# Optimization experiments

Hardware: AMD Instinct MI355X
Metric: run time of the kernel (lower is better)

The kernel has to match this reference:

```python
import jax, jax.numpy as jnp
import numpy as np

B, IN, E, D = 131072, 113, 4, 8
H1, H2 = 256, 113          # expert MLP dims [256, 113]
T1, T2 = 256, 128          # tower dims: fcn_dims = [256, 128]
EPS = 1e-5


def _bn(x, gamma, beta):
    # Training-mode BatchNorm1d over the batch axis (axis 0), biased variance.
    mean = jnp.mean(x, axis=0, keepdims=True)
    var = jnp.var(x, axis=0, keepdims=True)
    return (x - mean) * jax.lax.rsqrt(var + EPS) * gamma + beta


def setup_inputs() -> dict:
    key = jax.random.key(0)
    ks = jax.random.split(key, 24)
    s = 0.02
    return {
        "emb": jax.random.normal(ks[0], (B, IN), jnp.float32),
        "domain_id": jax.random.randint(ks[1], (B,), 0, D, jnp.int64),
        # experts (stacked over E): Linear->BN->ReLU, Linear->BN->ReLU
        "We1": jax.random.normal(ks[2], (E, IN, H1), jnp.float32) * s,
        "be1": jnp.zeros((E, H1), jnp.float32),
        "eg1": jnp.ones((E, H1), jnp.float32),
        "eb1": jnp.zeros((E, H1), jnp.float32),
        "We2": jax.random.normal(ks[3], (E, H1, H2), jnp.float32) * s,
        "be2": jnp.zeros((E, H2), jnp.float32),
        "eg2": jnp.ones((E, H2), jnp.float32),
        "eb2": jnp.zeros((E, H2), jnp.float32),
        # gates (stacked over D): Linear(IN, E) + softmax
        "Wg": jax.random.normal(ks[4], (D, IN, E), jnp.float32) * s,
        "bg": jnp.zeros((D, E), jnp.float32),
        # domain towers (stacked over D): 113->256 BN ReLU -> 128 BN ReLU -> 1, sigmoid
        "Wt1": jax.random.normal(ks[5], (D, H2, T1), jnp.float32) * s,
        "bt1": jnp.zeros((D, T1), jnp.float32),
        "tg1": jnp.ones((D, T1), jnp.float32),
        "tb1": jnp.zeros((D, T1), jnp.float32),
        "Wt2": jax.random.normal(ks[6], (D, T1, T2), jnp.float32) * s,
        "bt2": jnp.zeros((D, T2), jnp.float32),
        "tg2": jnp.ones((D, T2), jnp.float32),
        "tb2": jnp.zeros((D, T2), jnp.float32),
        "Wt3": jax.random.normal(ks[7], (D, T2, 1), jnp.float32) * s,
        "bt3": jnp.zeros((D, 1), jnp.float32),
    }


def reference(emb, We1, be1, eg1, eb1, We2, be2, eg2, eb2, Wg, bg,
              Wt1, bt1, tg1, tb1, Wt2, bt2, tg2, tb2, Wt3, bt3, domain_id):
    # experts, batched over E: [B, E, H1] -> [B, E, H2]
    h = jax.nn.relu(_bn(jnp.einsum('bi,eio->beo', emb, We1) + be1, eg1, eb1))
    fea = jax.nn.relu(_bn(jnp.einsum('beo,eoc->bec', h, We2) + be2, eg2, eb2))
    # gates, batched over D: [B, D, E] softmax over experts
    gates = jax.nn.softmax(jnp.einsum('bi,die->bde', emb, Wg) + bg, axis=-1)
    # soft mixture: [B, D, H2]
    task = jnp.einsum('bde,bec->bdc', gates, fea)
    # domain towers, batched over D (original computes every tower on the full batch)
    t1 = jax.nn.relu(_bn(jnp.einsum('bdc,dco->bdo', task, Wt1) + bt1, tg1, tb1))
    t2 = jax.nn.relu(_bn(jnp.einsum('bdo,doh->bdh', t1, Wt2) + bt2, tg2, tb2))
    out = jax.nn.sigmoid(jnp.einsum('bdh,dho->bdo', t2, Wt3) + bt3)[..., 0]  # [B, D]
    # masked select: final[b] = out[b, domain_id[b]]
    final = jnp.take_along_axis(out, domain_id[:, None], axis=1)[:, 0]  # [B]
    return final
```

## Files before the change

### kernel.cpp

```cpp
#include <hip/hip_runtime.h>
#include <hip/hip_bf16.h>


#define B_ROWS 131072
#define EPS_BN 1e-5f

typedef unsigned short bf_t;
typedef unsigned int u32;
typedef short bf16x8 __attribute__((ext_vector_type(8)));
typedef float f32x4  __attribute__((ext_vector_type(4)));

__device__ __forceinline__ float bf2f(bf_t u) { return __uint_as_float(((u32)u) << 16); }
__device__ __forceinline__ bf_t f2bf(float f) {
    u32 x = __float_as_uint(f);
    u32 r = x + 0x7FFFu + ((x >> 16) & 1u);
    return (bf_t)(r >> 16);
}

__global__ __launch_bounds__(256)
void prep_w(const float* __restrict__ W, bf_t* __restrict__ WT,
            int G, int K, int N, int CPAD, int KP)
{
    long total = (long)G * CPAD * KP;
    for (long idx = (long)blockIdx.x * 256 + threadIdx.x; idx < total;
         idx += (long)gridDim.x * 256) {
        int kk = (int)(idx % KP);
        long t = idx / KP;
        int c = (int)(t % CPAD);
        int g = (int)(t / CPAD);
        float v = 0.f;
        if (kk < K && c < N) v = W[((long)g * K + kk) * N + c];
        WT[idx] = f2bf(v);
    }
}

__global__ __launch_bounds__(256)
void prep_emb(const float* __restrict__ emb, bf_t* __restrict__ embB)
{
    const long total = (long)B_ROWS * 16;
    for (long idx = (long)blockIdx.x * 256 + threadIdx.x; idx < total;
         idx += (long)gridDim.x * 256) {
        long b = idx >> 4;
        int c0 = (int)(idx & 15) << 3;
        u32 o[4];
#pragma unroll
        for (int p = 0; p < 4; ++p) {
            int c = c0 + p * 2;
            float f0 = (c < 113)     ? emb[b * 113 + c]     : 0.f;
            float f1 = (c + 1 < 113) ? emb[b * 113 + c + 1] : 0.f;
            o[p] = (u32)f2bf(f0) | ((u32)f2bf(f1) << 16);
        }
        *(uint4*)&embB[b * 128 + c0] = make_uint4(o[0], o[1], o[2], o[3]);
    }
}

template<int XMODE, int NTILE, int KPAD, bool SEL>
__global__ __launch_bounds__(512, 1)
void gemm_big(const bf_t* __restrict__ X, int xrs, int Kreal,
              const float* __restrict__ gates,
              const float* __restrict__ statS, const float* __restrict__ statQ,
              const float* __restrict__ gamma, const float* __restrict__ beta, int nchIn,
              const bf_t* __restrict__ WT,
              const float* __restrict__ bias, int N,
              bf_t* __restrict__ Y, int yrs, int ycol0,
              const int* __restrict__ dom, int dsel,
              float* __restrict__ oSum, float* __restrict__ oSq)
{
    constexpr int NCH  = KPAD / 128;
    constexpr int WSTR = KPAD + 8;
    constexpr int XSTR = 136;
    constexpr int WCW  = NTILE / 4;
    constexpr int CF   = WCW / 16;
    constexpr int TPB  = 4;
    constexpr int NIT  = TPB * NCH;

    __shared__ bf_t  WsL[NTILE * WSTR];
    __shared__ bf_t  XsL[2][128 * XSTR];
    __shared__ float scS[512], shS[512];

    const int tid  = threadIdx.x;
    const int lane = tid & 63;
    const int w    = tid >> 6;
    const int wr   = w >> 2, wc = w & 3;
    const int g    = lane >> 4, lr = lane & 15;
    const int sr   = tid >> 2;
    const int so   = (tid & 3) << 5;
    const long tb0 = (long)blockIdx.x * TPB;

#pragma unroll
    for (int i = 0; i < NTILE * KPAD / 8 / 512; ++i) {
        int idx = tid + i * 512;
        int col = idx / (KPAD / 8);
        int ks  = (idx % (KPAD / 8)) * 8;
        *(uint4*)&WsL[col * WSTR + ks] = *(const uint4*)&WT[(long)col * KPAD + ks];
    }
    if (XMODE != 0) {
        for (int c = tid; c < nchIn; c += 512) {
            float m = statS[c] * (1.f / B_ROWS);
            float v = statQ[c] * (1.f / B_ROWS) - m * m;
            float s = gamma[c] * rsqrtf(v + EPS_BN);
            scS[c] = s;
            shS[c] = beta[c] - m * s;
        }
    }
    float bj[CF];
#pragma unroll
    for (int ci = 0; ci < CF; ++ci) {
        int col = wc * WCW + ci * 16 + lr;
        bj[ci] = (col < N) ? bias[col] : 0.f;
    }
    __syncthreads();

    f32x4 acc[4][CF];
#pragma unroll
    for (int ri = 0; ri < 4; ++ri)
#pragma unroll
        for (int ci = 0; ci < CF; ++ci) acc[ri][ci] = (f32x4){0.f, 0.f, 0.f, 0.f};
    float csum[CF], csq[CF];
#pragma unroll
    for (int ci = 0; ci < CF; ++ci) { csum[ci] = 0.f; csq[ci] = 0.f; }

    auto issue4 = [&](int it, uint4* r) {
        int t = it / NCH, ck = (it % NCH) << 7;
        long row = (tb0 + t) * 128 + sr;
#pragma unroll
        for (int j = 0; j < 4; ++j)
            r[j] = *(const uint4*)&X[row * (long)xrs + ck + so + j * 8];
    };
    auto twrite = [&](int it, const uint4* r) {
        bf_t* dst = &XsL[it & 1][sr * XSTR + so];
        if (XMODE == 0) {
#pragma unroll
            for (int j = 0; j < 4; ++j) *(uint4*)(dst + j * 8) = r[j];
        } else {
            int ck = (it % NCH) << 7;
#pragma unroll
            for (int j = 0; j < 4; ++j) {
                u32 q[4] = {r[j].x, r[j].y, r[j].z, r[j].w};
                u32 o[4];
#pragma unroll
                for (int p = 0; p < 4; ++p) {
                    int k0 = ck + so + j * 8 + p * 2;
                    float f0 = fmaxf(bf2f((bf_t)(q[p] & 0xffffu)) * scS[k0] + shS[k0], 0.f);
                    float f1 = fmaxf(bf2f((bf_t)(q[p] >> 16)) * scS[k0 + 1] + shS[k0 + 1], 0.f);
                    o[p] = (u32)f2bf(f0) | ((u32)f2bf(f1) << 16);
                }
                *(uint4*)(dst + j * 8) = make_uint4(o[0], o[1], o[2], o[3]);
            }
        }
    };
    auto stage2 = [&](int it) {
        long row = (tb0 + it) * 128 + sr;
        float4 g4 = *(const float4*)&gates[row * 32];
        uint4 r[16];
#pragma unroll
        for (int j = 0; j < 4; ++j)
#pragma unroll
            for (int e = 0; e < 4; ++e)
                r[j * 4 + e] = *(const uint4*)&X[row * 480 + e * 120 + so + j * 8];
        float ge[4] = {g4.x, g4.y, g4.z, g4.w};
        bf_t* dst = &XsL[it & 1][sr * XSTR + so];
#pragma unroll
        for (int j = 0; j < 4; ++j) {
            float vv[8];
#pragma unroll
            for (int p = 0; p < 8; ++p) vv[p] = 0.f;
#pragma unroll
            for (int e = 0; e < 4; ++e) {
                u32 q[4] = {r[j * 4 + e].x, r[j * 4 + e].y, r[j * 4 + e].z, r[j * 4 + e].w};
#pragma unroll
                for (int p = 0; p < 8; ++p) {
                    int k = so + j * 8 + p;
                    if (k < Kreal) {
                        float f = bf2f((bf_t)((q[p >> 1] >> ((p & 1) * 16)) & 0xffffu));
                        int ch = e * 113 + k;
                        f = fmaxf(f * scS[ch] + shS[ch], 0.f);
                        vv[p] = fmaf(ge[e], f, vv[p]);
                    }
                }
            }
            u32 o[4];
#pragma unroll
            for (int p = 0; p < 4; ++p)
                o[p] = (u32)f2bf(vv[p * 2]) | ((u32)f2bf(vv[p * 2 + 1]) << 16);
            *(uint4*)(dst + j * 8) = make_uint4(o[0], o[1], o[2], o[3]);
        }
    };
    auto do_mfma = [&](int it) {
        const bf_t* xb = XsL[it & 1];
        const int ck = (it % NCH) << 7;
#pragma unroll
        for (int kt = 0; kt < 4; ++kt) {
            bf16x8 af[4];
#pragma unroll
            for (int ri = 0; ri < 4; ++ri)
                af[ri] = *(const bf16x8*)&xb[(wr * 64 + ri * 16 + lr) * XSTR + kt * 32 + g * 8];
#pragma unroll
            for (int ci = 0; ci < CF; ++ci) {
                bf16x8 bf8 = *(const bf16x8*)&WsL[(wc * WCW + ci * 16 + lr) * WSTR + ck + kt * 32 + g * 8];
#pragma unroll
                for (int ri = 0; ri < 4; ++ri)
                    acc[ri][ci] = __builtin_amdgcn_mfma_f32_16x16x32_bf16(
                        af[ri], bf8, acc[ri][ci], 0, 0, 0);
            }
        }
    };
    auto epi = [&](int t) {
        const long row0 = (tb0 + t) * 128;
#pragma unroll
        for (int ci = 0; ci < CF; ++ci) {
            int col = wc * WCW + ci * 16 + lr;
            bool cv = col < N;
#pragma unroll
            for (int ri = 0; ri < 4; ++ri) {
#pragma unroll
                for (int reg = 0; reg < 4; ++reg) {
                    long row = row0 + wr * 64 + ri * 16 + g * 4 + reg;
                    float y = acc[ri][ci][reg] + bj[ci];
                    csum[ci] += y;
                    csq[ci]  += y * y;
                    bool st = cv;
                    if (SEL) st = st && (dom[row] == dsel);
                    if (st) Y[row * (long)yrs + ycol0 + col] = f2bf(y);
                    acc[ri][ci][reg] = 0.f;
                }
            }
        }
    };

    if (XMODE != 2) {
        uint4 rA[4], rB[4];
        issue4(0, rA);
#pragma unroll 1
        for (int ip = 0; ip < NIT; ip += 2) {
            if (ip + 1 < NIT) issue4(ip + 1, rB);
            twrite(ip, rA);
            __syncthreads();
            do_mfma(ip);
            if ((ip % NCH) == NCH - 1) epi(ip / NCH);
            if (ip + 2 < NIT) issue4(ip + 2, rA);
            twrite(ip + 1, rB);
            __syncthreads();
            do_mfma(ip + 1);
            if (((ip + 1) % NCH) == NCH - 1) epi((ip + 1) / NCH);
        }
    } else {
#pragma unroll 1
        for (int it = 0; it < NIT; ++it) {
            stage2(it);
            __syncthreads();
            do_mfma(it);
            epi(it);
        }
    }

#pragma unroll
    for (int ci = 0; ci < CF; ++ci) {
        float s = csum[ci], q = csq[ci];
        s += __shfl_xor(s, 16); s += __shfl_xor(s, 32);
        q += __shfl_xor(q, 16); q += __shfl_xor(q, 32);
        if (lane < 16) {
            int col = wc * WCW + ci * 16 + lane;
            if (col < N) {
                atomicAdd(&oSum[col], s);
                atomicAdd(&oSq[col], q);
            }
        }
    }
}

__global__ __launch_bounds__(256)
void gates_kernel(const float* __restrict__ emb, const float* __restrict__ Wg,
                  const float* __restrict__ bg, float* __restrict__ gates)
{
    __shared__ float embS[64][116];
    __shared__ float WgS[8 * 113 * 4];
    __shared__ float bgS[32];
    const int tid = threadIdx.x;
    const int r0 = blockIdx.x << 6;

    for (int idx = tid; idx < 64 * 113; idx += 256) {
        int rr = idx / 113, kk = idx - rr * 113;
        embS[rr][kk] = emb[(long)(r0 + rr) * 113 + kk];
    }
    for (int idx = tid; idx < 8 * 113 * 4; idx += 256) WgS[idx] = Wg[idx];
    if (tid < 32) bgS[tid] = bg[tid];
    __syncthreads();

    const int q = tid & 3;
    const int r = tid >> 2;
#pragma unroll
    for (int p = 0; p < 2; ++p) {
        int d = q + p * 4;
        float lg[4] = {bgS[d * 4 + 0], bgS[d * 4 + 1], bgS[d * 4 + 2], bgS[d * 4 + 3]};
        for (int k = 0; k < 113; ++k) {
            float x = embS[r][k];
            const float* wp = &WgS[(d * 113 + k) * 4];
#pragma unroll
            for (int e = 0; e < 4; ++e) lg[e] = fmaf(x, wp[e], lg[e]);
        }
        float m = fmaxf(fmaxf(lg[0], lg[1]), fmaxf(lg[2], lg[3]));
        float ex[4], s = 0.f;
#pragma unroll
        for (int e = 0; e < 4; ++e) { ex[e] = expf(lg[e] - m); s += ex[e]; }
        float inv = 1.f / s;
        *(float4*)&gates[(long)(r0 + r) * 32 + d * 4] =
            make_float4(ex[0] * inv, ex[1] * inv, ex[2] * inv, ex[3] * inv);
    }
}

__global__ __launch_bounds__(256)
void final_kernel(const bf_t* __restrict__ Y4d, const int* __restrict__ dom,
                  const float* __restrict__ s4sum, const float* __restrict__ s4sq,
                  const float* __restrict__ g4, const float* __restrict__ b4,
                  const float* __restrict__ w3, const float* __restrict__ b3,
                  int d, float* __restrict__ out)
{
    __shared__ float sc[128], sh[128], wS[128];
    const int tid = threadIdx.x;
    if (tid < 128) {
        float m = s4sum[tid] * (1.f / B_ROWS);
        float v = s4sq[tid] * (1.f / B_ROWS) - m * m;
        float s = g4[tid] * rsqrtf(v + EPS_BN);
        sc[tid] = s;
        sh[tid] = b4[tid] - m * s;
        wS[tid] = w3[tid];
    }
    __syncthreads();
    const float bb = b3[0];
    for (long b = (long)blockIdx.x * 256 + tid; b < B_ROWS; b += (long)gridDim.x * 256) {
        if ((dom[b] & 7) == d) {
            const bf_t* yp = Y4d + b * 128;
            float acc = bb;
            for (int c = 0; c < 128; c += 8) {
                uint4 raw = *(const uint4*)(yp + c);
                u32 w4[4] = {raw.x, raw.y, raw.z, raw.w};
#pragma unroll
                for (int j = 0; j < 8; ++j) {
                    float f = bf2f((bf_t)((w4[j >> 1] >> ((j & 1) * 16)) & 0xffffu));
                    float h = fmaxf(f * sc[c + j] + sh[c + j], 0.f);
                    acc = fmaf(h, wS[c + j], acc);
                }
            }
            out[b] = 1.f / (1.f + expf(-acc));
        }
    }
}

extern "C" void kernel_launch(void* const* d_in, const int* in_sizes, int n_in,
                              void* d_out, int out_size, void* d_ws, size_t ws_size,
                              hipStream_t stream)
{
    const float* emb = (const float*)d_in[0];
    const int*   dom = (const int*)d_in[1];
    const float* We1 = (const float*)d_in[2];
    const float* be1 = (const float*)d_in[3];
    const float* eg1 = (const float*)d_in[4];
    const float* eb1 = (const float*)d_in[5];
    const float* We2 = (const float*)d_in[6];
    const float* be2 = (const float*)d_in[7];
    const float* eg2 = (const float*)d_in[8];
    const float* eb2 = (const float*)d_in[9];
    const float* Wg  = (const float*)d_in[10];
    const float* bg  = (const float*)d_in[11];
    const float* Wt1 = (const float*)d_in[12];
    const float* bt1 = (const float*)d_in[13];
    const float* tg1 = (const float*)d_in[14];
    const float* tb1 = (const float*)d_in[15];
    const float* Wt2 = (const float*)d_in[16];
    const float* bt2 = (const float*)d_in[17];
    const float* tg2 = (const float*)d_in[18];
    const float* tb2 = (const float*)d_in[19];
    const float* Wt3 = (const float*)d_in[20];
    const float* bt3 = (const float*)d_in[21];
    float* out = (float*)d_out;

    char* ws = (char*)d_ws;
    bf_t*  Y2    = (bf_t*)(ws);
    float* gates = (float*)(ws + 125829120LL);
    bf_t*  Yx    = (bf_t*)(ws + 142606336LL);
    bf_t*  Y4    = (bf_t*)(ws + 209715200LL);
    float* S     = (float*)(ws + 243269632LL);
    bf_t*  WTa   = (bf_t*)(ws + 243306496LL);

    bf_t* embB = Y4;
    bf_t* We1T = WTa;
    bf_t* We2T = We1T + 131072;
    bf_t* Wt1T = We2T + 131072;
    bf_t* Wt2T = Wt1T + 262144;

    float* S1s = S;           float* S1q = S1s + 1024;
    float* S2s = S1q + 1024;  float* S2q = S2s + 452;
    float* S3s = S2q + 452;   float* S3q = S3s + 2048;
    float* S4s = S3q + 2048;  float* S4q = S4s + 1024;

    hipMemsetAsync(S, 0, 9096 * sizeof(float), stream);

    prep_w<<<512, 256, 0, stream>>>(We1, We1T, 4, 113, 256, 256, 128);
    prep_w<<<512, 256, 0, stream>>>(We2, We2T, 4, 256, 113, 128, 256);
    prep_w<<<1024, 256, 0, stream>>>(Wt1, Wt1T, 8, 113, 256, 256, 128);
    prep_w<<<1024, 256, 0, stream>>>(Wt2, Wt2T, 8, 256, 128, 128, 256);
    prep_emb<<<2048, 256, 0, stream>>>(emb, embB);

    gates_kernel<<<2048, 256, 0, stream>>>(emb, Wg, bg, gates);

    for (int e = 0; e < 4; ++e) {
        gemm_big<0, 256, 128, false><<<256, 512, 0, stream>>>(
            embB, 128, 128,
            nullptr, nullptr, nullptr, nullptr, nullptr, 0,
            We1T + (long)e * 32768,
            be1 + e * 256, 256,
            Yx, 256, 0, nullptr, 0, S1s + e * 256, S1q + e * 256);
        gemm_big<1, 128, 256, false><<<256, 512, 0, stream>>>(
            Yx, 256, 256,
            nullptr, S1s + e * 256, S1q + e * 256, eg1 + e * 256, eb1 + e * 256, 256,
            We2T + (long)e * 32768,
            be2 + e * 113, 113,
            Y2, 480, e * 120, nullptr, 0, S2s + e * 113, S2q + e * 113);
    }

    for (int d = 0; d < 8; ++d) {
        gemm_big<2, 256, 128, false><<<256, 512, 0, stream>>>(
            Y2, 480, 113,
            gates + d * 4, S2s, S2q, eg2, eb2, 452,
            Wt1T + (long)d * 32768,
            bt1 + d * 256, 256,
            Yx, 256, 0, nullptr, 0, S3s + d * 256, S3q + d * 256);
        gemm_big<1, 128, 256, true><<<256, 512, 0, stream>>>(
            Yx, 256, 256,
            nullptr, S3s + d * 256, S3q + d * 256, tg1 + d * 256, tb1 + d * 256, 256,
            Wt2T + (long)d * 32768,
            bt2 + d * 128, 128,
            Y4, 128, 0, dom, d, S4s + d * 128, S4q + d * 128);
        final_kernel<<<1024, 256, 0, stream>>>(
            Y4, dom, S4s + d * 128, S4q + d * 128,
            tg2 + d * 128, tb2 + d * 128, Wt3 + d * 128, bt3 + d, d, out);
    }

    (void)in_sizes; (void)n_in; (void)out_size; (void)ws_size;
}
```

Measured before the change: 1.788 ms.

## Keep GEMM weight fragments in registers and XOR-swizzle the activation LDS tile

Each thread now loads its B-operand weight fragments for the whole K range into registers once per block, instead of staging the weight tile in shared memory and re-reading it for every MFMA step. The activation tile in LDS drops its padded stride and uses an XOR swizzle on 16-byte chunks to avoid bank conflicts. This removes the weight LDS traffic and shrinks LDS usage. In exchange it raises register pressure a lot, since CF*KT bf16x8 fragments stay live, which may cause spills for the wider NOUT/KPAD instances.

```diff
diff --git a/kernel.cpp b/kernel.cpp
--- a/kernel.cpp
+++ b/kernel.cpp
@@ -54,28 +54,26 @@
     }
 }
 
-template<int XMODE, int NTILE, int KPAD, bool SEL>
+template<int XMODE, int NOUT, int KPAD, bool SEL>
 __global__ __launch_bounds__(512, 1)
 void gemm_big(const bf_t* __restrict__ X, int xrs, int Kreal,
               const float* __restrict__ gates,
               const float* __restrict__ statS, const float* __restrict__ statQ,
               const float* __restrict__ gamma, const float* __restrict__ beta, int nchIn,
               const bf_t* __restrict__ WT,
-              const float* __restrict__ bias, int N,
+              const float* __restrict__ bias, int Nvalid,
               bf_t* __restrict__ Y, int yrs, int ycol0,
               const int* __restrict__ dom, int dsel,
               float* __restrict__ oSum, float* __restrict__ oSq)
 {
-    constexpr int NCH  = KPAD / 128;
-    constexpr int WSTR = KPAD + 8;
-    constexpr int XSTR = 136;
-    constexpr int WCW  = NTILE / 4;
-    constexpr int CF   = WCW / 16;
-    constexpr int TPB  = 4;
-    constexpr int NIT  = TPB * NCH;
-
-    __shared__ bf_t  WsL[NTILE * WSTR];
-    __shared__ bf_t  XsL[2][128 * XSTR];
+    constexpr int WCW = NOUT / 4;
+    constexpr int CF  = WCW / 16;
+    constexpr int KT  = KPAD / 32;
+    constexpr int NCH = KPAD / 128;
+    constexpr int TPB = 4;
+    constexpr int NIT = TPB * NCH;
+
+    __shared__ bf_t  XsL[2][128 * 128];
     __shared__ float scS[512], shS[512];
 
     const int tid  = threadIdx.x;
@@ -84,15 +82,16 @@
     const int wr   = w >> 2, wc = w & 3;
     const int g    = lane >> 4, lr = lane & 15;
     const int sr   = tid >> 2;
-    const int so   = (tid & 3) << 5;
+    const int sq   = tid & 3;
     const long tb0 = (long)blockIdx.x * TPB;
 
-#pragma unroll
-    for (int i = 0; i < NTILE * KPAD / 8 / 512; ++i) {
-        int idx = tid + i * 512;
-        int col = idx / (KPAD / 8);
-        int ks  = (idx % (KPAD / 8)) * 8;
-        *(uint4*)&WsL[col * WSTR + ks] = *(const uint4*)&WT[(long)col * KPAD + ks];
+    bf16x8 bw[CF][KT];
+#pragma unroll
+    for (int ci = 0; ci < CF; ++ci) {
+        const bf_t* wp = WT + (long)(wc * WCW + ci * 16 + lr) * KPAD + g * 8;
+#pragma unroll
+        for (int kt = 0; kt < KT; ++kt)
+            bw[ci][kt] = *(const bf16x8*)(wp + kt * 32);
     }
     if (XMODE != 0) {
         for (int c = tid; c < nchIn; c += 512) {
@@ -107,7 +106,7 @@
 #pragma unroll
     for (int ci = 0; ci < CF; ++ci) {
         int col = wc * WCW + ci * 16 + lr;
-        bj[ci] = (col < N) ? bias[col] : 0.f;
+        bj[ci] = (col < Nvalid) ? bias[col] : 0.f;
     }
     __syncthreads();
 
@@ -120,89 +119,94 @@
 #pragma unroll
     for (int ci = 0; ci < CF; ++ci) { csum[ci] = 0.f; csq[ci] = 0.f; }
 
+    auto ldsw = [&](int buf, int j) -> char* {
+        int byte = (sr << 8) + (sq << 6) + (j << 4);
+        byte ^= (sr & 7) << 4;
+        return (char*)XsL[buf] + byte;
+    };
     auto issue4 = [&](int it, uint4* r) {
         int t = it / NCH, ck = (it % NCH) << 7;
-        long row = (tb0 + t) * 128 + sr;
-#pragma unroll
-        for (int j = 0; j < 4; ++j)
-            r[j] = *(const uint4*)&X[row * (long)xrs + ck + so + j * 8];
+        const bf_t* p = X + ((tb0 + t) * 128 + sr) * (long)xrs + ck + (sq << 5);
+#pragma unroll
+        for (int j = 0; j < 4; ++j) r[j] = *(const uint4*)(p + j * 8);
     };
     auto twrite = [&](int it, const uint4* r) {
-        bf_t* dst = &XsL[it & 1][sr * XSTR + so];
+        int buf = it & 1;
         if (XMODE == 0) {
 #pragma unroll
-            for (int j = 0; j < 4; ++j) *(uint4*)(dst + j * 8) = r[j];
+            for (int j = 0; j < 4; ++j) *(uint4*)ldsw(buf, j) = r[j];
         } else {
-            int ck = (it % NCH) << 7;
+            int kb = ((it % NCH) << 7) + (sq << 5);
 #pragma unroll
             for (int j = 0; j < 4; ++j) {
                 u32 q[4] = {r[j].x, r[j].y, r[j].z, r[j].w};
                 u32 o[4];
 #pragma unroll
-                for (int p = 0; p < 4; ++p) {
-                    int k0 = ck + so + j * 8 + p * 2;
-                    float f0 = fmaxf(bf2f((bf_t)(q[p] & 0xffffu)) * scS[k0] + shS[k0], 0.f);
-                    float f1 = fmaxf(bf2f((bf_t)(q[p] >> 16)) * scS[k0 + 1] + shS[k0 + 1], 0.f);
-                    o[p] = (u32)f2bf(f0) | ((u32)f2bf(f1) << 16);
+                for (int p2 = 0; p2 < 4; ++p2) {
+                    int k0 = kb + j * 8 + p2 * 2;
+                    float f0 = fmaxf(bf2f((bf_t)(q[p2] & 0xffffu)) * scS[k0] + shS[k0], 0.f);
+                    float f1 = fmaxf(bf2f((bf_t)(q[p2] >> 16)) * scS[k0 + 1] + shS[k0 + 1], 0.f);
+                    o[p2] = (u32)f2bf(f0) | ((u32)f2bf(f1) << 16);
                 }
-                *(uint4*)(dst + j * 8) = make_uint4(o[0], o[1], o[2], o[3]);
+                *(uint4*)ldsw(buf, j) = make_uint4(o[0], o[1], o[2], o[3]);
             }
         }
     };
     auto stage2 = [&](int it) {
         long row = (tb0 + it) * 128 + sr;
-        float4 g4 = *(const float4*)&gates[row * 32];
-        uint4 r[16];
-#pragma unroll
-        for (int j = 0; j < 4; ++j)
+        float4 g4v = *(const float4*)&gates[row * 32];
+        float ge[4] = {g4v.x, g4v.y, g4v.z, g4v.w};
+        int buf = it & 1;
+#pragma unroll
+        for (int j = 0; j < 4; ++j) {
+            int kb = (sq << 5) + j * 8;
+            uint4 re[4];
 #pragma unroll
             for (int e = 0; e < 4; ++e)
-                r[j * 4 + e] = *(const uint4*)&X[row * 480 + e * 120 + so + j * 8];
-        float ge[4] = {g4.x, g4.y, g4.z, g4.w};
-        bf_t* dst = &XsL[it & 1][sr * XSTR + so];
-#pragma unroll
-        for (int j = 0; j < 4; ++j) {
+                re[e] = *(const uint4*)&X[row * 480 + e * 120 + kb];
             float vv[8];
 #pragma unroll
-            for (int p = 0; p < 8; ++p) vv[p] = 0.f;
+            for (int p2 = 0; p2 < 8; ++p2) vv[p2] = 0.f;
 #pragma unroll
             for (int e = 0; e < 4; ++e) {
-                u32 q[4] = {r[j * 4 + e].x, r[j * 4 + e].y, r[j * 4 + e].z, r[j * 4 + e].w};
-#pragma unroll
-                for (int p = 0; p < 8; ++p) {
-                    int k = so + j * 8 + p;
+                u32 q[4] = {re[e].x, re[e].y, re[e].z, re[e].w};
+#pragma unroll
+                for (int p2 = 0; p2 < 8; ++p2) {
+                    int k = kb + p2;
                     if (k < Kreal) {
-                        float f = bf2f((bf_t)((q[p >> 1] >> ((p & 1) * 16)) & 0xffffu));
+                        float f = bf2f((bf_t)((q[p2 >> 1] >> ((p2 & 1) * 16)) & 0xffffu));
                         int ch = e * 113 + k;
                         f = fmaxf(f * scS[ch] + shS[ch], 0.f);
-                        vv[p] = fmaf(ge[e], f, vv[p]);
+                        vv[p2] = fmaf(ge[e], f, vv[p2]);
                     }
                 }
             }
             u32 o[4];
 #pragma unroll
-            for (int p = 0; p < 4; ++p)
-                o[p] = (u32)f2bf(vv[p * 2]) | ((u32)f2bf(vv[p * 2 + 1]) << 16);
-            *(uint4*)(dst + j * 8) = make_uint4(o[0], o[1], o[2], o[3]);
+            for (int p2 = 0; p2 < 4; ++p2)
+                o[p2] = (u32)f2bf(vv[p2 * 2]) | ((u32)f2bf(vv[p2 * 2 + 1]) << 16);
+            *(uint4*)ldsw(buf, j) = make_uint4(o[0], o[1], o[2], o[3]);
         }
     };
     auto do_mfma = [&](int it) {
-        const bf_t* xb = XsL[it & 1];
-        const int ck = (it % NCH) << 7;
+        const char* xb = (const char*)XsL[it & 1];
+        const int kg0 = (it % NCH) * 4;
 #pragma unroll
         for (int kt = 0; kt < 4; ++kt) {
             bf16x8 af[4];
 #pragma unroll
-            for (int ri = 0; ri < 4; ++ri)
-                af[ri] = *(const bf16x8*)&xb[(wr * 64 + ri * 16 + lr) * XSTR + kt * 32 + g * 8];
-#pragma unroll
-            for (int ci = 0; ci < CF; ++ci) {
-                bf16x8 bf8 = *(const bf16x8*)&WsL[(wc * WCW + ci * 16 + lr) * WSTR + ck + kt * 32 + g * 8];
+            for (int ri = 0; ri < 4; ++ri) {
+                int row = wr * 64 + ri * 16 + lr;
+                int byte = (row << 8) + (kt << 6) + (g << 4);
+                byte ^= (lr & 7) << 4;
+                af[ri] = *(const bf16x8*)(xb + byte);
+            }
+#pragma unroll
+            for (int ci = 0; ci < CF; ++ci)
 #pragma unroll
                 for (int ri = 0; ri < 4; ++ri)
                     acc[ri][ci] = __builtin_amdgcn_mfma_f32_16x16x32_bf16(
-                        af[ri], bf8, acc[ri][ci], 0, 0, 0);
-            }
+                        af[ri], bw[ci][kg0 + kt], acc[ri][ci], 0, 0, 0);
         }
     };
     auto epi = [&](int t) {
@@ -210,7 +214,7 @@
 #pragma unroll
         for (int ci = 0; ci < CF; ++ci) {
             int col = wc * WCW + ci * 16 + lr;
-            bool cv = col < N;
+            bool cv = col < Nvalid;
 #pragma unroll
             for (int ri = 0; ri < 4; ++ri) {
 #pragma unroll
@@ -261,7 +265,7 @@
         q += __shfl_xor(q, 16); q += __shfl_xor(q, 32);
         if (lane < 16) {
             int col = wc * WCW + ci * 16 + lane;
-            if (col < N) {
+            if (col < Nvalid) {
                 atomicAdd(&oSum[col], s);
                 atomicAdd(&oSq[col], q);
             }
```

Result: slower. 2.059 ms (+15.2%).
